# Kernel tuning notes

Hardware: AMD Instinct MI355X
Metric: run time of the kernel (lower is better)

The kernel has to match this reference:

```python
import jax, jax.numpy as jnp
import numpy as np

INPUT_SIZE = 1024
HIDDEN_SIZE = 1024
BATCH = 16384


def _linear_params(key, out_dim, in_dim):
    # torch nn.Linear init: U(-1/sqrt(in_dim), 1/sqrt(in_dim))
    kw, kb = jax.random.split(key)
    bound = 1.0 / np.sqrt(in_dim)
    W = jax.random.uniform(kw, (out_dim, in_dim), jnp.float32, -bound, bound)
    b = jax.random.uniform(kb, (out_dim,), jnp.float32, -bound, bound)
    return W, b


def setup_inputs() -> dict:
    key = jax.random.key(0)
    ks = jax.random.split(key, 9)
    x = jax.random.normal(ks[0], (BATCH, INPUT_SIZE), jnp.float32)
    h = jax.random.normal(ks[1], (BATCH, HIDDEN_SIZE), jnp.float32)
    c = jax.random.normal(ks[2], (BATCH, HIDDEN_SIZE), jnp.float32)
    W_ii, b_ii = _linear_params(ks[3], HIDDEN_SIZE, INPUT_SIZE)
    W_hi, b_hi = _linear_params(ks[4], HIDDEN_SIZE, HIDDEN_SIZE)
    W_if, b_if = _linear_params(ks[5], HIDDEN_SIZE, INPUT_SIZE)
    W_hf, b_hf = _linear_params(ks[6], HIDDEN_SIZE, HIDDEN_SIZE)
    W_ig, b_ig = _linear_params(ks[7], HIDDEN_SIZE, INPUT_SIZE)
    W_hg, b_hg = _linear_params(ks[8], HIDDEN_SIZE, HIDDEN_SIZE)
    return {"x": x, "h": h, "c": c,
            "W_ii": W_ii, "b_ii": b_ii, "W_hi": W_hi, "b_hi": b_hi,
            "W_if": W_if, "b_if": b_if, "W_hf": W_hf, "b_hf": b_hf,
            "W_ig": W_ig, "b_ig": b_ig, "W_hg": W_hg, "b_hg": b_hg}


def reference(x, h, c, W_ii, b_ii, W_hi, b_hi, W_if, b_if, W_hf, b_hf,
              W_ig, b_ig, W_hg, b_hg):
    # Fuse the three x-projections and three h-projections into two wide GEMMs.
    Wx = jnp.concatenate([W_ii, W_if, W_ig], axis=0)   # [3H, I]
    Wh = jnp.concatenate([W_hi, W_hf, W_hg], axis=0)   # [3H, H]
    bx = jnp.concatenate([b_ii, b_if, b_ig], axis=0)   # [3H]
    bh = jnp.concatenate([b_hi, b_hf, b_hg], axis=0)   # [3H]
    gates = x @ Wx.T + bx + h @ Wh.T + bh               # [B, 3H]
    gi, gf, gg = jnp.split(gates, 3, axis=-1)
    i_t = jax.nn.sigmoid(gi)
    f_t = jax.nn.sigmoid(gf)
    c_tilde = jnp.tanh(gg)
    new_c = f_t * c + i_t * c_tilde
    return new_c
```

## Files before the change

kernel.cpp:

```cpp
#include <hip/hip_runtime.h>


#define HS      1024
#define K_TOTAL 2048
#define NKT     32
#define A_TILE  16384
#define W_TILE  24576
#define BUFB    40960

typedef __bf16 bf16;
typedef bf16  bf16x4  __attribute__((ext_vector_type(4)));
typedef bf16  bf16x8  __attribute__((ext_vector_type(8)));
typedef float f32x4   __attribute__((ext_vector_type(4)));
typedef float f32x16  __attribute__((ext_vector_type(16)));

__device__ __forceinline__ void cp16(void* lds, const void* g) {
  __builtin_amdgcn_global_load_lds(
      (const __attribute__((address_space(1))) void*)g,
      (__attribute__((address_space(3))) void*)lds, 16, 0, 0);
}

__device__ __forceinline__ bf16x8 cvt8(const f32x4 v0, const f32x4 v1) {
  bf16x8 o;
  o[0] = (bf16)v0[0]; o[1] = (bf16)v0[1]; o[2] = (bf16)v0[2]; o[3] = (bf16)v0[3];
  o[4] = (bf16)v1[0]; o[5] = (bf16)v1[1]; o[6] = (bf16)v1[2]; o[7] = (bf16)v1[3];
  return o;
}

__global__ __launch_bounds__(256) void pack_a(const float* __restrict__ x,
                                              const float* __restrict__ h,
                                              bf16* __restrict__ Aws) {
  const unsigned gt   = blockIdx.x * 256 + threadIdx.x;
  const unsigned Lb   = gt * 16;
  const unsigned tile = Lb >> 14;
  const unsigned o    = Lb & 16383u;
  const unsigned row  = o >> 7;
  const unsigned kb   = (o & 127u) ^ ((row & 7u) << 4);
  const unsigned mt   = tile >> 5;
  const unsigned kt   = tile & 31u;
  const unsigned m    = mt * 128 + row;
  const unsigned kg   = kt * 64 + (kb >> 1);
  const float* src = (kg < 1024u) ? (x + (size_t)m * HS + kg)
                                  : (h + (size_t)m * HS + (kg - 1024u));
  const f32x4 v0 = *(const f32x4*)src;
  const f32x4 v1 = *(const f32x4*)(src + 4);
  *(bf16x8*)((char*)Aws + Lb) = cvt8(v0, v1);
}

__global__ __launch_bounds__(256) void pack_w(
    const float* __restrict__ w_ii, const float* __restrict__ w_hi,
    const float* __restrict__ w_if, const float* __restrict__ w_hf,
    const float* __restrict__ w_ig, const float* __restrict__ w_hg,
    bf16* __restrict__ Wws) {
  const unsigned gt  = blockIdx.x * 256 + threadIdx.x;
  const unsigned Lb  = gt * 16;
  const unsigned nt  = Lb / 786432u;
  const unsigned r1  = Lb % 786432u;
  const unsigned kt  = r1 / 24576u;
  const unsigned r2  = r1 % 24576u;
  const unsigned g   = r2 >> 13;
  const unsigned o   = r2 & 8191u;
  const unsigned row = o >> 7;
  const unsigned kb  = (o & 127u) ^ ((row & 7u) << 4);
  const unsigned n   = nt * 64 + row;
  const unsigned kg  = kt * 64 + (kb >> 1);
  const float* wx = (g == 0) ? w_ii : (g == 1) ? w_if : w_ig;
  const float* wh = (g == 0) ? w_hi : (g == 1) ? w_hf : w_hg;
  const float* src = (kg < 1024u) ? (wx + (size_t)n * HS + kg)
                                  : (wh + (size_t)n * HS + (kg - 1024u));
  const f32x4 v0 = *(const f32x4*)src;
  const f32x4 v1 = *(const f32x4*)(src + 4);
  *(bf16x8*)((char*)Wws + Lb) = cvt8(v0, v1);
}

__global__ __launch_bounds__(256, 2) void lstm_gemm(
    const bf16* __restrict__ Aws, const bf16* __restrict__ Wws,
    const float* __restrict__ c,
    const float* __restrict__ b_ii, const float* __restrict__ b_hi,
    const float* __restrict__ b_if, const float* __restrict__ b_hf,
    const float* __restrict__ b_ig, const float* __restrict__ b_hg,
    float* __restrict__ out)
{
  __shared__ __align__(16) char smem[2 * BUFB];

  const int tid  = threadIdx.x;
  const int lane = tid & 63;
  const int wave = tid >> 6;

  const int bid = blockIdx.x;
  const int wg  = (bid & 7) * 256 + (bid >> 3);
  const int nt  = wg & 15;
  const int mt  = wg >> 4;
  const int m0  = mt * 128;
  const int n0  = nt * 64;
  const int wm  = (wave & 1) * 64;
  const int wn  = (wave >> 1) * 32;

  const char* Apan = (const char*)Aws + (size_t)mt * (NKT * A_TILE);
  const char* Wpan = (const char*)Wws + (size_t)nt * (NKT * W_TILE);

  const int aoff = wave * 4 * 1024;
  const int boff = wave * 6 * 1024;
  const int lb   = lane * 16;

  f32x16 acc[3][2] = {};

  auto stage = [&](int t, int sel) {
    char* bufA = smem + sel * BUFB;
    char* bufB = bufA + A_TILE;
    const char* At = Apan + t * A_TILE + aoff + lb;
    const char* Wt = Wpan + (size_t)t * W_TILE + boff + lb;
#pragma unroll
    for (int i = 0; i < 4; ++i) cp16(bufA + aoff + i * 1024, At + i * 1024);
#pragma unroll
    for (int i = 0; i < 6; ++i) cp16(bufB + boff + i * 1024, Wt + i * 1024);
  };

  stage(0, 0);
  __syncthreads();

  const int fr    = lane & 31;
  const int fk8b  = (lane >> 5) * 16;
  const int xr    = (fr & 7) << 4;

  for (int t = 0; t < NKT; ++t) {
    if (t < NKT - 1) stage(t + 1, (t + 1) & 1);

    const char* bufA  = smem + (t & 1) * BUFB;
    const char* bufB  = bufA + A_TILE;
    const char* arow0 = bufA + (wm + fr) * 128;
    const char* arow1 = bufA + (wm + 32 + fr) * 128;
    const char* brow  = bufB + (wn + fr) * 128;

#pragma unroll
    for (int ks = 0; ks < 4; ++ks) {
      const int kb = (ks * 32 + fk8b) ^ xr;
      const bf16x8 a0 = *(const bf16x8*)(arow0 + kb);
      const bf16x8 a1 = *(const bf16x8*)(arow1 + kb);
#pragma unroll
      for (int g = 0; g < 3; ++g) {
        const bf16x8 b = *(const bf16x8*)(brow + g * 8192 + kb);
        acc[g][0] = __builtin_amdgcn_mfma_f32_32x32x16_bf16(a0, b, acc[g][0], 0, 0, 0);
        acc[g][1] = __builtin_amdgcn_mfma_f32_32x32x16_bf16(a1, b, acc[g][1], 0, 0, 0);
      }
    }
    __syncthreads();
  }

  const int n   = n0 + wn + (lane & 31);
  const int rb  = (lane >> 5) * 4;
  const float bi  = b_ii[n] + b_hi[n];
  const float bf_ = b_if[n] + b_hf[n];
  const float bg  = b_ig[n] + b_hg[n];
#pragma unroll
  for (int i = 0; i < 2; ++i) {
#pragma unroll
    for (int r = 0; r < 16; ++r) {
      const int m = m0 + wm + i * 32 + (r & 3) + 8 * (r >> 2) + rb;
      const size_t idx = (size_t)m * HS + n;
      const float gi = acc[0][i][r] + bi;
      const float gf = acc[1][i][r] + bf_;
      const float gg = acc[2][i][r] + bg;
      const float it = 1.f / (1.f + __expf(-gi));
      const float ft = 1.f / (1.f + __expf(-gf));
      const float e2 = __expf(-2.f * gg);
      const float gt = (1.f - e2) / (1.f + e2);
      out[idx] = ft * c[idx] + it * gt;
    }
  }
}

#define BK      32
#define NITER   (K_TOTAL / BK)

__device__ __forceinline__ void ldpanel(const float* __restrict__ src, int tid,
                                        f32x4* __restrict__ v) {
#pragma unroll
  for (int b = 0; b < 2; ++b) {
    const int cc  = tid + b * 256;
    const int row = cc >> 3;
    const int col = (cc & 7) * 4;
    v[b] = *(const f32x4*)(src + (size_t)row * HS + col);
  }
}

__device__ __forceinline__ void stpanel(bf16* __restrict__ dst, int tid,
                                        const f32x4* __restrict__ v) {
#pragma unroll
  for (int b = 0; b < 2; ++b) {
    const int cc  = tid + b * 256;
    const int row = cc >> 3;
    const int col = (cc & 7) * 4;
    bf16x4 o;
    o[0] = (bf16)v[b][0]; o[1] = (bf16)v[b][1];
    o[2] = (bf16)v[b][2]; o[3] = (bf16)v[b][3];
    *(bf16x4*)(dst + row * 32 + col) = o;
  }
}

__device__ __forceinline__ void get_srcs(
    int k, int m0, int n0,
    const float* __restrict__ x, const float* __restrict__ h,
    const float* __restrict__ w_ii, const float* __restrict__ w_hi,
    const float* __restrict__ w_if, const float* __restrict__ w_hf,
    const float* __restrict__ w_ig, const float* __restrict__ w_hg,
    const float* s[5]) {
  const int kk = k * BK;
  const float* Ag; const float* w0; const float* w1; const float* w2; int kl;
  if (kk < 1024) { Ag = x; w0 = w_ii; w1 = w_if; w2 = w_ig; kl = kk; }
  else           { Ag = h; w0 = w_hi; w1 = w_hf; w2 = w_hg; kl = kk - 1024; }
  s[0] = Ag + (size_t)m0 * HS + kl;
  s[1] = Ag + (size_t)(m0 + 64) * HS + kl;
  s[2] = w0 + (size_t)n0 * HS + kl;
  s[3] = w1 + (size_t)n0 * HS + kl;
  s[4] = w2 + (size_t)n0 * HS + kl;
}

__global__ __launch_bounds__(256, 2) void lstm_fused(
    const float* __restrict__ x, const float* __restrict__ h,
    const float* __restrict__ c,
    const float* __restrict__ w_ii, const float* __restrict__ w_hi,
    const float* __restrict__ w_if, const float* __restrict__ w_hf,
    const float* __restrict__ w_ig, const float* __restrict__ w_hg,
    const float* __restrict__ b_ii, const float* __restrict__ b_hi,
    const float* __restrict__ b_if, const float* __restrict__ b_hf,
    const float* __restrict__ b_ig, const float* __restrict__ b_hg,
    float* __restrict__ out)
{
  __shared__ bf16 smem[2 * 10240];

  const int tid  = threadIdx.x;
  const int lane = tid & 63;
  const int wave = tid >> 6;

  const int bid = blockIdx.x;
  const int nt  = bid & 15;
  const int mt  = bid >> 4;
  const int m0  = mt * 128;
  const int n0  = nt * 64;
  const int wm  = (wave & 1) * 64;
  const int wn  = (wave >> 1) * 32;

  f32x16 acc[3][2] = {};

  {
    const float* s[5];
    get_srcs(0, m0, n0, x, h, w_ii, w_hi, w_if, w_hf, w_ig, w_hg, s);
    f32x4 pf[5][2];
#pragma unroll
    for (int p = 0; p < 5; ++p) ldpanel(s[p], tid, pf[p]);
    bf16* A0 = smem;
#pragma unroll
    for (int p = 0; p < 5; ++p) stpanel(A0 + p * 2048, tid, pf[p]);
    __syncthreads();
  }

  const int fr  = lane & 31;
  const int fk8 = (lane >> 5) * 8;

  for (int k = 0; k < NITER; ++k) {
    bf16* As = smem + (k & 1) * 10240;
    bf16* Bs = As + 4096;

    f32x4 nf[5][2];
    if (k < NITER - 1) {
      const float* s[5];
      get_srcs(k + 1, m0, n0, x, h, w_ii, w_hi, w_if, w_hf, w_ig, w_hg, s);
#pragma unroll
      for (int p = 0; p < 5; ++p) ldpanel(s[p], tid, nf[p]);
    }

#pragma unroll
    for (int ks = 0; ks < 2; ++ks) {
      const int co = ks * 16 + fk8;
      bf16x8 a0 = *(const bf16x8*)(As + (wm + fr) * 32 + co);
      bf16x8 a1 = *(const bf16x8*)(As + (wm + 32 + fr) * 32 + co);
#pragma unroll
      for (int g = 0; g < 3; ++g) {
        bf16x8 b = *(const bf16x8*)(Bs + g * 2048 + (wn + fr) * 32 + co);
        acc[g][0] = __builtin_amdgcn_mfma_f32_32x32x16_bf16(a0, b, acc[g][0], 0, 0, 0);
        acc[g][1] = __builtin_amdgcn_mfma_f32_32x32x16_bf16(a1, b, acc[g][1], 0, 0, 0);
      }
    }

    if (k < NITER - 1) {
      bf16* An = smem + ((k + 1) & 1) * 10240;
#pragma unroll
      for (int p = 0; p < 5; ++p) stpanel(An + p * 2048, tid, nf[p]);
    }
    __syncthreads();
  }

  const int n   = n0 + wn + (lane & 31);
  const int rb  = (lane >> 5) * 4;
  const float bi  = b_ii[n] + b_hi[n];
  const float bf_ = b_if[n] + b_hf[n];
  const float bg  = b_ig[n] + b_hg[n];
#pragma unroll
  for (int i = 0; i < 2; ++i) {
#pragma unroll
    for (int r = 0; r < 16; ++r) {
      const int m = m0 + wm + i * 32 + (r & 3) + 8 * (r >> 2) + rb;
      const size_t idx = (size_t)m * HS + n;
      const float gi = acc[0][i][r] + bi;
      const float gf = acc[1][i][r] + bf_;
      const float gg = acc[2][i][r] + bg;
      const float it = 1.f / (1.f + __expf(-gi));
      const float ft = 1.f / (1.f + __expf(-gf));
      const float e2 = __expf(-2.f * gg);
      const float gt = (1.f - e2) / (1.f + e2);
      out[idx] = ft * c[idx] + it * gt;
    }
  }
}

extern "C" void kernel_launch(void* const* d_in, const int* in_sizes, int n_in,
                              void* d_out, int out_size, void* d_ws, size_t ws_size,
                              hipStream_t stream) {
  const float* x  = (const float*)d_in[0];
  const float* h  = (const float*)d_in[1];
  const float* c  = (const float*)d_in[2];
  const float* w_ii = (const float*)d_in[3];
  const float* b_ii = (const float*)d_in[4];
  const float* w_hi = (const float*)d_in[5];
  const float* b_hi = (const float*)d_in[6];
  const float* w_if = (const float*)d_in[7];
  const float* b_if = (const float*)d_in[8];
  const float* w_hf = (const float*)d_in[9];
  const float* b_hf = (const float*)d_in[10];
  const float* w_ig = (const float*)d_in[11];
  const float* b_ig = (const float*)d_in[12];
  const float* w_hg = (const float*)d_in[13];
  const float* b_hg = (const float*)d_in[14];
  float* out = (float*)d_out;

  const size_t needA = (size_t)16384 * 2048 * 2;
  const size_t needW = (size_t)3 * 1024 * 2048 * 2;

  if (ws_size >= needA + needW) {
    bf16* Aws = (bf16*)d_ws;
    bf16* Wws = (bf16*)((char*)d_ws + needA);
    hipLaunchKernelGGL(pack_a, dim3(16384), dim3(256), 0, stream, x, h, Aws);
    hipLaunchKernelGGL(pack_w, dim3(3072), dim3(256), 0, stream,
                       w_ii, w_hi, w_if, w_hf, w_ig, w_hg, Wws);
    hipLaunchKernelGGL(lstm_gemm, dim3(2048), dim3(256), 0, stream,
                       Aws, Wws, c, b_ii, b_hi, b_if, b_hf, b_ig, b_hg, out);
  } else {
    hipLaunchKernelGGL(lstm_fused, dim3(2048), dim3(256), 0, stream,
                       x, h, c, w_ii, w_hi, w_if, w_hf, w_ig, w_hg,
                       b_ii, b_hi, b_if, b_hf, b_ig, b_hg, out);
  }
}
```

Measured before the change: 446.5 us.

## Repack operands in MFMA fragment order and deepen LDS pipeline to four half-tiles

The pack kernels now write A and W in per-lane MFMA fragment order instead of swizzled row-major tiles, so each wave reads its operands from LDS with a lane-contiguous 16-byte load and no XOR addressing. The GEMM main loop splits each K tile into two halves and keeps a four-buffer ring with three stages in flight. It synchronises with explicit vmcnt waits plus a bare barrier in place of __syncthreads, and raises wave priority around the MFMA block. This aims to hide global-to-LDS latency and cut LDS bank conflicts and address math, at the cost of the same total LDS and more delicate hand-written wait counts.

```diff
diff --git a/kernel.cpp b/kernel.cpp
--- a/kernel.cpp
+++ b/kernel.cpp
@@ -3,10 +3,12 @@
 
 #define HS      1024
 #define K_TOTAL 2048
-#define NKT     32
-#define A_TILE  16384
-#define W_TILE  24576
-#define BUFB    40960
+#define NHALF   64
+#define AH_B    8192
+#define WH_B    12288
+#define BUFB    20480
+#define A_MT_B  524288
+#define W_NT_B  786432
 
 typedef __bf16 bf16;
 typedef bf16  bf16x4  __attribute__((ext_vector_type(4)));
@@ -14,6 +16,8 @@
 typedef float f32x4   __attribute__((ext_vector_type(4)));
 typedef float f32x16  __attribute__((ext_vector_type(16)));
 
+#define WAITVM(N) asm volatile("s_waitcnt vmcnt(" #N ")" ::: "memory")
+
 __device__ __forceinline__ void cp16(void* lds, const void* g) {
   __builtin_amdgcn_global_load_lds(
       (const __attribute__((address_space(1))) void*)g,
@@ -31,20 +35,20 @@
                                               const float* __restrict__ h,
                                               bf16* __restrict__ Aws) {
   const unsigned gt   = blockIdx.x * 256 + threadIdx.x;
-  const unsigned Lb   = gt * 16;
-  const unsigned tile = Lb >> 14;
-  const unsigned o    = Lb & 16383u;
-  const unsigned row  = o >> 7;
-  const unsigned kb   = (o & 127u) ^ ((row & 7u) << 4);
-  const unsigned mt   = tile >> 5;
-  const unsigned kt   = tile & 31u;
-  const unsigned m    = mt * 128 + row;
-  const unsigned kg   = kt * 64 + (kb >> 1);
-  const float* src = (kg < 1024u) ? (x + (size_t)m * HS + kg)
-                                  : (h + (size_t)m * HS + (kg - 1024u));
+  const unsigned byte = gt * 16;
+  const unsigned mt   = byte >> 19;
+  const unsigned kt   = (byte >> 14) & 31u;
+  const unsigned half = (byte >> 13) & 1u;
+  const unsigned frag = (byte >> 10) & 7u;
+  const unsigned lane = (byte >> 4) & 63u;
+  const unsigned m  = mt * 128 + (frag >> 1) * 32 + (lane & 31u);
+  const unsigned ks = half * 2 + (frag & 1u);
+  const unsigned k  = kt * 64 + ks * 16 + (lane >> 5) * 8;
+  const float* src = (k < 1024u) ? (x + (size_t)m * HS + k)
+                                 : (h + (size_t)m * HS + (k - 1024u));
   const f32x4 v0 = *(const f32x4*)src;
   const f32x4 v1 = *(const f32x4*)(src + 4);
-  *(bf16x8*)((char*)Aws + Lb) = cvt8(v0, v1);
+  *(bf16x8*)((char*)Aws + byte) = cvt8(v0, v1);
 }
 
 __global__ __launch_bounds__(256) void pack_w(
@@ -52,25 +56,28 @@
     const float* __restrict__ w_if, const float* __restrict__ w_hf,
     const float* __restrict__ w_ig, const float* __restrict__ w_hg,
     bf16* __restrict__ Wws) {
-  const unsigned gt  = blockIdx.x * 256 + threadIdx.x;
-  const unsigned Lb  = gt * 16;
-  const unsigned nt  = Lb / 786432u;
-  const unsigned r1  = Lb % 786432u;
-  const unsigned kt  = r1 / 24576u;
-  const unsigned r2  = r1 % 24576u;
-  const unsigned g   = r2 >> 13;
-  const unsigned o   = r2 & 8191u;
-  const unsigned row = o >> 7;
-  const unsigned kb  = (o & 127u) ^ ((row & 7u) << 4);
-  const unsigned n   = nt * 64 + row;
-  const unsigned kg  = kt * 64 + (kb >> 1);
+  const unsigned gt   = blockIdx.x * 256 + threadIdx.x;
+  const unsigned byte = gt * 16;
+  const unsigned nt = byte / 786432u;
+  const unsigned r  = byte % 786432u;
+  const unsigned kt = r / 24576u;
+  const unsigned r2 = r % 24576u;
+  const unsigned half = (r2 >= 12288u) ? 1u : 0u;
+  const unsigned r3 = r2 - half * 12288u;
+  const unsigned frag = r3 >> 10;
+  const unsigned lane = (r3 >> 4) & 63u;
+  const unsigned g    = frag >> 2;
+  const unsigned n32  = (frag >> 1) & 1u;
+  const unsigned ks   = half * 2 + (frag & 1u);
+  const unsigned n = nt * 64 + n32 * 32 + (lane & 31u);
+  const unsigned k = kt * 64 + ks * 16 + (lane >> 5) * 8;
   const float* wx = (g == 0) ? w_ii : (g == 1) ? w_if : w_ig;
   const float* wh = (g == 0) ? w_hi : (g == 1) ? w_hf : w_hg;
-  const float* src = (kg < 1024u) ? (wx + (size_t)n * HS + kg)
-                                  : (wh + (size_t)n * HS + (kg - 1024u));
+  const float* src = (k < 1024u) ? (wx + (size_t)n * HS + k)
+                                 : (wh + (size_t)n * HS + (k - 1024u));
   const f32x4 v0 = *(const f32x4*)src;
   const f32x4 v1 = *(const f32x4*)(src + 4);
-  *(bf16x8*)((char*)Wws + Lb) = cvt8(v0, v1);
+  *(bf16x8*)((char*)Wws + byte) = cvt8(v0, v1);
 }
 
 __global__ __launch_bounds__(256, 2) void lstm_gemm(
@@ -81,7 +88,7 @@
     const float* __restrict__ b_ig, const float* __restrict__ b_hg,
     float* __restrict__ out)
 {
-  __shared__ __align__(16) char smem[2 * BUFB];
+  __shared__ __align__(16) char smem[4 * BUFB];
 
   const int tid  = threadIdx.x;
   const int lane = tid & 63;
@@ -95,56 +102,63 @@
   const int n0  = nt * 64;
   const int wm  = (wave & 1) * 64;
   const int wn  = (wave >> 1) * 32;
-
-  const char* Apan = (const char*)Aws + (size_t)mt * (NKT * A_TILE);
-  const char* Wpan = (const char*)Wws + (size_t)nt * (NKT * W_TILE);
-
-  const int aoff = wave * 4 * 1024;
-  const int boff = wave * 6 * 1024;
+  const int r32a = (wave & 1) * 2;
+  const int n32  = (wave >> 1);
+
+  const char* Apan = (const char*)Aws + (size_t)mt * A_MT_B;
+  const char* Wpan = (const char*)Wws + (size_t)nt * W_NT_B;
+
+  const int aoff = wave * 2048;
+  const int boff = wave * 3072;
   const int lb   = lane * 16;
 
   f32x16 acc[3][2] = {};
 
-  auto stage = [&](int t, int sel) {
-    char* bufA = smem + sel * BUFB;
-    char* bufB = bufA + A_TILE;
-    const char* At = Apan + t * A_TILE + aoff + lb;
-    const char* Wt = Wpan + (size_t)t * W_TILE + boff + lb;
-#pragma unroll
-    for (int i = 0; i < 4; ++i) cp16(bufA + aoff + i * 1024, At + i * 1024);
-#pragma unroll
-    for (int i = 0; i < 6; ++i) cp16(bufB + boff + i * 1024, Wt + i * 1024);
+  auto stage = [&](int h, int buf) {
+    char* dst = smem + buf * BUFB;
+    const char* sa = Apan + (size_t)h * AH_B + aoff + lb;
+    const char* sw = Wpan + (size_t)h * WH_B + boff + lb;
+    cp16(dst + aoff,        sa);
+    cp16(dst + aoff + 1024, sa + 1024);
+    char* dw = dst + AH_B + boff;
+    cp16(dw,        sw);
+    cp16(dw + 1024, sw + 1024);
+    cp16(dw + 2048, sw + 2048);
   };
 
   stage(0, 0);
-  __syncthreads();
-
-  const int fr    = lane & 31;
-  const int fk8b  = (lane >> 5) * 16;
-  const int xr    = (fr & 7) << 4;
-
-  for (int t = 0; t < NKT; ++t) {
-    if (t < NKT - 1) stage(t + 1, (t + 1) & 1);
-
-    const char* bufA  = smem + (t & 1) * BUFB;
-    const char* bufB  = bufA + A_TILE;
-    const char* arow0 = bufA + (wm + fr) * 128;
-    const char* arow1 = bufA + (wm + 32 + fr) * 128;
-    const char* brow  = bufB + (wn + fr) * 128;
-
-#pragma unroll
-    for (int ks = 0; ks < 4; ++ks) {
-      const int kb = (ks * 32 + fk8b) ^ xr;
-      const bf16x8 a0 = *(const bf16x8*)(arow0 + kb);
-      const bf16x8 a1 = *(const bf16x8*)(arow1 + kb);
-#pragma unroll
-      for (int g = 0; g < 3; ++g) {
-        const bf16x8 b = *(const bf16x8*)(brow + g * 8192 + kb);
-        acc[g][0] = __builtin_amdgcn_mfma_f32_32x32x16_bf16(a0, b, acc[g][0], 0, 0, 0);
-        acc[g][1] = __builtin_amdgcn_mfma_f32_32x32x16_bf16(a1, b, acc[g][1], 0, 0, 0);
-      }
-    }
-    __syncthreads();
+  stage(1, 1);
+  stage(2, 2);
+
+#pragma unroll 4
+  for (int h = 0; h < NHALF; ++h) {
+    if (h < NHALF - 2)      { WAITVM(10); }
+    else if (h == NHALF - 2){ WAITVM(5);  }
+    else                    { WAITVM(0);  }
+    __builtin_amdgcn_s_barrier();
+
+    if (h < NHALF - 3) stage(h + 3, (h + 3) & 3);
+
+    const char* base = smem + (h & 3) * BUFB;
+    const char* Ab = base + lb;
+    const char* Wb = base + AH_B + lb;
+
+#pragma unroll
+    for (int ks2 = 0; ks2 < 2; ++ks2) {
+      const bf16x8 a0 = *(const bf16x8*)(Ab + (((r32a    ) * 2 + ks2) << 10));
+      const bf16x8 a1 = *(const bf16x8*)(Ab + (((r32a + 1) * 2 + ks2) << 10));
+      const bf16x8 b0 = *(const bf16x8*)(Wb + (((0 * 2 + n32) * 2 + ks2) << 10));
+      const bf16x8 b1 = *(const bf16x8*)(Wb + (((1 * 2 + n32) * 2 + ks2) << 10));
+      const bf16x8 b2 = *(const bf16x8*)(Wb + (((2 * 2 + n32) * 2 + ks2) << 10));
+      __builtin_amdgcn_s_setprio(1);
+      acc[0][0] = __builtin_amdgcn_mfma_f32_32x32x16_bf16(a0, b0, acc[0][0], 0, 0, 0);
+      acc[0][1] = __builtin_amdgcn_mfma_f32_32x32x16_bf16(a1, b0, acc[0][1], 0, 0, 0);
+      acc[1][0] = __builtin_amdgcn_mfma_f32_32x32x16_bf16(a0, b1, acc[1][0], 0, 0, 0);
+      acc[1][1] = __builtin_amdgcn_mfma_f32_32x32x16_bf16(a1, b1, acc[1][1], 0, 0, 0);
+      acc[2][0] = __builtin_amdgcn_mfma_f32_32x32x16_bf16(a0, b2, acc[2][0], 0, 0, 0);
+      acc[2][1] = __builtin_amdgcn_mfma_f32_32x32x16_bf16(a1, b2, acc[2][1], 0, 0, 0);
+      __builtin_amdgcn_s_setprio(0);
+    }
   }
 
   const int n   = n0 + wn + (lane & 31);
@@ -334,8 +348,8 @@
   const float* b_hg = (const float*)d_in[14];
   float* out = (float*)d_out;
 
-  const size_t needA = (size_t)16384 * 2048 * 2;
-  const size_t needW = (size_t)3 * 1024 * 2048 * 2;
+  const size_t needA = (size_t)128 * A_MT_B;
+  const size_t needW = (size_t)16 * W_NT_B;
 
   if (ws_size >= needA + needW) {
     bf16* Aws = (bf16*)d_ws;
```

Measured after the change: 456.1 us. 2.2% more time.
